# Optimization experiments

Measured on AMD Instinct MI355X. Metric: run time of the kernel, lower is better.

The kernel has to match this reference:

```python
import jax, jax.numpy as jnp
import numpy as np
from jax import lax

K = 5       # pool kernel
S = 2       # pool stride
POOL_FEATS = 36  # 6*6 pooled map flattened


def setup_inputs() -> dict:
    key = jax.random.key(0)
    k1, k2, k3 = jax.random.split(key, 3)
    B, C, H, W_ = 256, 512, 16, 16
    x = jax.random.normal(k1, (B, C, H, W_), dtype=jnp.float32)
    # shared Linear(36, 1): weight [1, 36], bias [1] (torch default-like init)
    lim = 1.0 / np.sqrt(POOL_FEATS)
    W = jax.random.uniform(k2, (1, POOL_FEATS), dtype=jnp.float32, minval=-lim, maxval=lim)
    b = jax.random.uniform(k3, (1,), dtype=jnp.float32, minval=-lim, maxval=lim)
    return {"x": x, "W": W, "b": b}


def _avgpool_5x5_s2(x):
    # x: [B, C, H, W] -> [B, C, 6, 6]; AvgPool2d(kernel=5, stride=2, pad=0)
    summed = lax.reduce_window(x, 0.0, lax.add,
                               window_dimensions=(1, 1, K, K),
                               window_strides=(1, 1, S, S),
                               padding='VALID')
    return summed / (K * K)


def reference(x, W, b):
    B, C = x.shape[0], x.shape[1]
    pooled = _avgpool_5x5_s2(x)                 # [B, C, 6, 6]
    feats = pooled.reshape(B, C, POOL_FEATS)    # [B, C, 36]
    # shared Linear(36,1) across all channels -> [B, C]
    out = jnp.einsum('bcf,of->bc', feats, W) + b[0]
    return out
```

## Files before the change

### kernel.cpp

```cpp
#include <hip/hip_runtime.h>


#define CH_TOTAL (256 * 512)
#define BLOCK 256

__global__ __launch_bounds__(BLOCK) void pool_linear_kernel(
    const float* __restrict__ x,
    const float* __restrict__ Wv,
    const float* __restrict__ bv,
    float* __restrict__ out)
{
    const int lane   = threadIdx.x & 63;
    const int waveId = (int)((blockIdx.x * blockDim.x + threadIdx.x) >> 6);
    const int nWaves = (int)((gridDim.x * blockDim.x) >> 6);

    float c[4];
#pragma unroll
    for (int j = 0; j < 4; ++j) {
        const int p = lane * 4 + j;
        const int h = p >> 4;
        const int w = p & 15;
        const int oh0 = max(0, (h - 3) / 2);
        const int oh1 = min(5, h >> 1);
        const int ow0 = max(0, (w - 3) / 2);
        const int ow1 = min(5, w >> 1);
        float s = 0.0f;
        for (int oh = oh0; oh <= oh1; ++oh)
            for (int ow = ow0; ow <= ow1; ++ow)
                s += Wv[oh * 6 + ow];
        c[j] = s * 0.04f;
    }
    const float bias = bv[0];

    const float4* __restrict__ x4 = reinterpret_cast<const float4*>(x);

    for (int ch = waveId; ch < CH_TOTAL; ch += nWaves) {
        const float4 v = x4[ch * 64 + lane];
        float part = v.x * c[0] + v.y * c[1] + v.z * c[2] + v.w * c[3];
#pragma unroll
        for (int off = 32; off > 0; off >>= 1)
            part += __shfl_down(part, off, 64);
        if (lane == 0) out[ch] = part + bias;
    }
}

extern "C" void kernel_launch(void* const* d_in, const int* in_sizes, int n_in,
                              void* d_out, int out_size, void* d_ws, size_t ws_size,
                              hipStream_t stream) {
    const float* x   = (const float*)d_in[0];
    const float* Wv  = (const float*)d_in[1];
    const float* bv  = (const float*)d_in[2];
    float* out       = (float*)d_out;

    pool_linear_kernel<<<dim3(2048), dim3(BLOCK), 0, stream>>>(x, Wv, bv, out);
}
```

Before: 194.4 us.

## Process 16 channels per wave with 16-lane groups and batched loads

Replaces the grid-stride loop, which handled one channel per wave per iteration, with a one-shot mapping: each wave handles 16 channels, split across 4 lane groups of 16, and issues 16 independent float4 loads before reducing. The grid is sized from the input so every wave does a fixed chunk. The goal is more memory-level parallelism and fewer shuffle reduction steps per channel (4 instead of 6). In exchange it uses more registers for the 16 float4 buffers and 16 coefficients, and the launch now has many more blocks.

```diff
diff --git a/kernel.cpp b/kernel.cpp
--- a/kernel.cpp
+++ b/kernel.cpp
@@ -1,46 +1,69 @@
 #include <hip/hip_runtime.h>
 
 
-#define CH_TOTAL (256 * 512)
 #define BLOCK 256
 
 __global__ __launch_bounds__(BLOCK) void pool_linear_kernel(
     const float* __restrict__ x,
     const float* __restrict__ Wv,
     const float* __restrict__ bv,
-    float* __restrict__ out)
+    float* __restrict__ out,
+    int nCh)
 {
+    const int tid    = blockIdx.x * BLOCK + threadIdx.x;
+    const int waveId = tid >> 6;
     const int lane   = threadIdx.x & 63;
-    const int waveId = (int)((blockIdx.x * blockDim.x + threadIdx.x) >> 6);
-    const int nWaves = (int)((gridDim.x * blockDim.x) >> 6);
+    const int g      = lane >> 4;
+    const int j      = lane & 15;
 
-    float c[4];
+    const int chBase = waveId * 16;
+    if (chBase >= nCh) return;
+
+    float c[4][4];
 #pragma unroll
-    for (int j = 0; j < 4; ++j) {
-        const int p = lane * 4 + j;
-        const int h = p >> 4;
-        const int w = p & 15;
-        const int oh0 = max(0, (h - 3) / 2);
-        const int oh1 = min(5, h >> 1);
-        const int ow0 = max(0, (w - 3) / 2);
-        const int ow1 = min(5, w >> 1);
-        float s = 0.0f;
-        for (int oh = oh0; oh <= oh1; ++oh)
-            for (int ow = ow0; ow <= ow1; ++ow)
-                s += Wv[oh * 6 + ow];
-        c[j] = s * 0.04f;
+    for (int q = 0; q < 4; ++q) {
+#pragma unroll
+        for (int k = 0; k < 4; ++k) {
+            const int p = (q * 16 + j) * 4 + k;
+            const int h = p >> 4;
+            const int w = p & 15;
+            const int oh0 = max(0, (h - 3) / 2);
+            const int oh1 = min(5, h >> 1);
+            const int ow0 = max(0, (w - 3) / 2);
+            const int ow1 = min(5, w >> 1);
+            float s = 0.0f;
+            for (int oh = oh0; oh <= oh1; ++oh)
+                for (int ow = ow0; ow <= ow1; ++ow)
+                    s += Wv[oh * 6 + ow];
+            c[q][k] = s * 0.04f;
+        }
     }
     const float bias = bv[0];
 
     const float4* __restrict__ x4 = reinterpret_cast<const float4*>(x);
 
-    for (int ch = waveId; ch < CH_TOTAL; ch += nWaves) {
-        const float4 v = x4[ch * 64 + lane];
-        float part = v.x * c[0] + v.y * c[1] + v.z * c[2] + v.w * c[3];
+    float4 v[4][4];
 #pragma unroll
-        for (int off = 32; off > 0; off >>= 1)
-            part += __shfl_down(part, off, 64);
-        if (lane == 0) out[ch] = part + bias;
+    for (int qp = 0; qp < 4; ++qp) {
+        const int ch = chBase + qp * 4 + g;
+#pragma unroll
+        for (int q = 0; q < 4; ++q)
+            v[qp][q] = x4[ch * 64 + q * 16 + j];
+    }
+
+#pragma unroll
+    for (int qp = 0; qp < 4; ++qp) {
+        float part = 0.0f;
+#pragma unroll
+        for (int q = 0; q < 4; ++q) {
+            part += v[qp][q].x * c[q][0] + v[qp][q].y * c[q][1]
+                  + v[qp][q].z * c[q][2] + v[qp][q].w * c[q][3];
+        }
+        part += __shfl_down(part, 8, 16);
+        part += __shfl_down(part, 4, 16);
+        part += __shfl_down(part, 2, 16);
+        part += __shfl_down(part, 1, 16);
+        if (j == 0) out[chBase + qp * 4 + g] = part + bias;
     }
 }
 
@@ -52,5 +75,9 @@
     const float* bv  = (const float*)d_in[2];
     float* out       = (float*)d_out;
 
-    pool_linear_kernel<<<dim3(2048), dim3(BLOCK), 0, stream>>>(x, Wv, bv, out);
+    const int nCh    = in_sizes[0] / 256;
+    const int waves  = (nCh + 15) / 16;
+    const int blocks = (waves + 3) / 4;
+
+    pool_linear_kernel<<<dim3(blocks), dim3(BLOCK), 0, stream>>>(x, Wv, bv, out, nCh);
 }
```

Result: slower. 206.4 us (+6.2%).
